# Performance work log

Measured on AMD Instinct MI355X. Metric: run time of the kernel, lower is better.

The kernel has to match this reference:

```python
import jax, jax.numpy as jnp
import numpy as np

N_NODES = 50000
N_EDGES = 1_600_000
D_IN, D_HID, D_OUT, K = 128, 50, 10, 5


def setup_inputs() -> dict:
    key = jax.random.key(0)
    ks = jax.random.split(key, 6)
    x = jax.random.normal(ks[0], (N_NODES, D_IN), dtype=jnp.float32)
    edge_index = jax.random.randint(ks[1], (2, N_EDGES), 0, N_NODES, dtype=jnp.int64)
    cheb_w = jax.random.normal(ks[2], (K, D_IN, D_HID), dtype=jnp.float32) * 0.05
    cheb_b = jax.random.normal(ks[3], (D_HID,), dtype=jnp.float32) * 0.05
    fc_w = jax.random.normal(ks[4], (D_HID, D_OUT), dtype=jnp.float32) * 0.1
    fc_b = jax.random.normal(ks[5], (D_OUT,), dtype=jnp.float32) * 0.1
    return {"x": x, "edge_index": edge_index, "cheb_w": cheb_w,
            "cheb_b": cheb_b, "fc_w": fc_w, "fc_b": fc_b}


def reference(x, edge_index, cheb_w, cheb_b, fc_w, fc_b):
    # ChebConv (PyG, normalization='sym', lambda_max=2.0):
    # L_hat = 2L/lambda_max - I = -D^{-1/2} A D^{-1/2} (zero diagonal)
    row, col = edge_index[0], edge_index[1]
    n = x.shape[0]
    deg = jax.ops.segment_sum(jnp.ones_like(row, dtype=x.dtype), row, num_segments=n)
    dinv = jnp.where(deg > 0, jax.lax.rsqrt(jnp.maximum(deg, 1.0)), 0.0)
    w = -dinv[row] * dinv[col]  # [E] edge weights of L_hat

    def prop(h):  # L_hat @ h via gather-scale-scatter
        return jax.ops.segment_sum(w[:, None] * h[col], row, num_segments=n)

    tx0 = x
    tx1 = prop(x)
    out = jnp.einsum('ni,io->no', tx0, cheb_w[0]) + jnp.einsum('ni,io->no', tx1, cheb_w[1])
    for k in range(2, K):
        tx2 = 2.0 * prop(tx1) - tx0
        out = out + jnp.einsum('ni,io->no', tx2, cheb_w[k])
        tx0, tx1 = tx1, tx2
    out = out + cheb_b

    h = jax.nn.relu(out)
    logits = h @ fc_w + fc_b
    return jax.nn.log_softmax(logits, axis=1)
```

## Files before the change

### kernel.cpp

```cpp
#include <hip/hip_runtime.h>
#include <hip/hip_fp16.h>

#define N_NODES 50000
#define N_EDGES 1600000
#define D_IN    128
#define D_HID   50
#define D_OUT   10
#define K_CHEB  5

#define WH_ELEMS  (K_CHEB * 64 * D_IN)
#define WH_BLOCKS ((WH_ELEMS + 255) / 256)
#define XH_BLOCKS (N_NODES * D_IN / 8 / 256)

#define P1S_BLOCKS 512
#define EPB        (N_EDGES / P1S_BLOCKS)
#define NBUCK      256
#define NB_USED    196
#define BCAP       48

#define VROW      64
#define VSTRIDE   ((size_t)(N_NODES + 1) * VROW)

#define NGROUP    (N_NODES / 16)
#define VG_SPAN   512
#define VG_WAVES  (K_CHEB * VG_SPAN)
#define VGB_BLOCKS (VG_WAVES / 8)

typedef _Float16 half8_t __attribute__((ext_vector_type(8)));
typedef float    f32x4_t __attribute__((ext_vector_type(4)));


__global__ __launch_bounds__(256) void buildA_kernel(const int* __restrict__ row,
                                                     const int* __restrict__ col,
                                                     unsigned int* __restrict__ store,
                                                     int* __restrict__ bcnt,
                                                     const float* __restrict__ x,
                                                     const float* __restrict__ W,
                                                     __half* __restrict__ xh,
                                                     __half* __restrict__ Wh,
                                                     __half* __restrict__ u,
                                                     __half* __restrict__ b1,
                                                     __half* __restrict__ b3,
                                                     __half* __restrict__ b2,
                                                     float* __restrict__ dinv) {
    __shared__ int cnt[NBUCK];
    int tid = threadIdx.x;
    int blk = blockIdx.x;
    if (blk < P1S_BLOCKS) {
        cnt[tid] = 0;
        __syncthreads();
        int base = blk * EPB;
        size_t sb = (size_t)blk * (NBUCK * BCAP);
        for (int i = tid; i < EPB; i += 256) {
            int r = row[base + i];
            int c = col[base + i];
            int b = r >> 8;
            int pos = atomicAdd(&cnt[b], 1);
            if (pos >= BCAP) pos = BCAP - 1;
            store[sb + b * BCAP + pos] = ((unsigned int)(r & 255) << 16) | (unsigned int)c;
        }
        __syncthreads();
        bcnt[blk * NBUCK + tid] = cnt[tid];
        return;
    }
    int pb = blk - P1S_BLOCKS;
    if (pb < XH_BLOCKS) {
        size_t base = ((size_t)pb * 256 + tid) * 8;
        float4 a = *(const float4*)(x + base);
        float4 b = *(const float4*)(x + base + 4);
        half8_t h;
        h[0] = (_Float16)a.x; h[1] = (_Float16)a.y;
        h[2] = (_Float16)a.z; h[3] = (_Float16)a.w;
        h[4] = (_Float16)b.x; h[5] = (_Float16)b.y;
        h[6] = (_Float16)b.z; h[7] = (_Float16)b.w;
        *(half8_t*)(xh + base) = h;
    } else if (pb < XH_BLOCKS + WH_BLOCKS) {
        int idx = (pb - XH_BLOCKS) * 256 + tid;
        if (idx < WH_ELEMS) {
            int i = idx & 127;
            int n = (idx >> 7) & 63;
            int t = idx >> 13;
            float vv = (n < D_HID) ? W[t * D_IN * D_HID + i * D_HID + n] : 0.f;
            Wh[idx] = __float2half(vv);
        }
    } else {
        if (tid < VROW) {
            __half z = __float2half(0.f);
            u[4 * VSTRIDE + (size_t)N_NODES * VROW + tid] = z;
            b1[(size_t)N_NODES * VROW + tid] = z;
            b3[(size_t)N_NODES * VROW + tid] = z;
            b2[(size_t)N_NODES * VROW + tid] = z;
        }
        if (tid == 64) dinv[N_NODES] = 0.f;
    }
}

__global__ __launch_bounds__(512) void buildB_kernel(const unsigned int* __restrict__ store,
                                                     const int* __restrict__ bcnt,
                                                     int* __restrict__ row_start,
                                                     float* __restrict__ dinv,
                                                     float* __restrict__ dinv2,
                                                     float* __restrict__ sdeg,
                                                     int* __restrict__ ewc,
                                                     const __half* __restrict__ xh,
                                                     const __half* __restrict__ Wh,
                                                     __half* __restrict__ u) {
    __shared__ int hist[256];
    __shared__ int off[256];
    __shared__ int fill[256];
    __shared__ int sb_part[512];
    __shared__ int pscan[256];
    __shared__ int s_bbase;
    int tid = threadIdx.x;
    int blk = blockIdx.x;
    if (blk >= NB_USED) {
        int lane = tid & 63;
        int wv = __builtin_amdgcn_readfirstlane(tid >> 6);
        int w = (blk - NB_USED) * 8 + wv;
        int t = w / VG_SPAN;
        int idx = w - t * VG_SPAN;
        int m = lane & 15;
        int quad = lane >> 4;

        const __half* Wt = Wh + t * (64 * D_IN);
        half8_t afr[4][4];
        #pragma unroll
        for (int ks = 0; ks < 4; ++ks) {
            int ko = ks * 32 + quad * 8;
            #pragma unroll
            for (int jt = 0; jt < 4; ++jt)
                afr[ks][jt] = *(const half8_t*)(Wt + (jt * 16 + m) * D_IN + ko);
        }

        __half* ut = u + t * VSTRIDE;

        half8_t pf[4];
        int g = idx;
        {
            const __half* xr = xh + (size_t)(g * 16 + m) * D_IN;
            #pragma unroll
            for (int ks = 0; ks < 4; ++ks)
                pf[ks] = *(const half8_t*)(xr + ks * 32 + quad * 8);
        }

        for (; g < NGROUP; g += VG_SPAN) {
            int node = g * 16 + m;
            half8_t bfr[4];
            #pragma unroll
            for (int ks = 0; ks < 4; ++ks) bfr[ks] = pf[ks];
            int gn = g + VG_SPAN;
            if (gn < NGROUP) {
                const __half* xr = xh + (size_t)(gn * 16 + m) * D_IN;
                #pragma unroll
                for (int ks = 0; ks < 4; ++ks)
                    pf[ks] = *(const half8_t*)(xr + ks * 32 + quad * 8);
            }
            f32x4_t acc[4];
            #pragma unroll
            for (int jt = 0; jt < 4; ++jt) acc[jt] = (f32x4_t)0.f;
            #pragma unroll
            for (int ks = 0; ks < 4; ++ks)
                #pragma unroll
                for (int jt = 0; jt < 4; ++jt)
                    acc[jt] = __builtin_amdgcn_mfma_f32_16x16x32_f16(afr[ks][jt], bfr[ks], acc[jt], 0, 0, 0);
            __half* dst = ut + (size_t)node * VROW + quad * 4;
            #pragma unroll
            for (int jt = 0; jt < 4; ++jt) {
                __half2 h0 = __float22half2_rn(make_float2(acc[jt][0], acc[jt][1]));
                __half2 h1 = __float22half2_rn(make_float2(acc[jt][2], acc[jt][3]));
                uint2 uu;
                uu.x = *(unsigned int*)&h0;
                uu.y = *(unsigned int*)&h1;
                *(uint2*)(dst + jt * 16) = uu;
            }
        }
        return;
    }
    int b = blk;
    {
        int bt = tid & 255, seg = tid >> 8;
        int sum = 0;
        for (int s = seg * 256; s < seg * 256 + 256; ++s) sum += bcnt[s * NBUCK + bt];
        sb_part[tid] = sum;
    }
    __syncthreads();
    if (tid < 256) pscan[tid] = sb_part[tid] + sb_part[256 + tid];
    __syncthreads();
    for (int o = 1; o < 256; o <<= 1) {
        int vv = (tid < 256 && tid >= o) ? pscan[tid - o] : 0;
        __syncthreads();
        if (tid < 256) pscan[tid] += vv;
        __syncthreads();
    }
    if (tid == 0) {
        s_bbase = (b == 0) ? 0 : pscan[b - 1];
        if (b == 0) row_start[N_NODES] = pscan[255];
    }
    if (tid < 256) hist[tid] = 0;
    __syncthreads();
    int bbase_b = s_bbase;

    int strip = tid;
    int sn = bcnt[strip * NBUCK + b];
    size_t sb = (size_t)strip * (NBUCK * BCAP) + b * BCAP;
    for (int i = 0; i < sn; ++i)
        atomicAdd(&hist[store[sb + i] >> 16], 1);
    __syncthreads();
    int d = (tid < 256) ? hist[tid] : 0;
    if (tid < 256) off[tid] = d;
    __syncthreads();
    for (int o = 1; o < 256; o <<= 1) {
        int vv = (tid < 256 && tid >= o) ? off[tid - o] : 0;
        __syncthreads();
        if (tid < 256) off[tid] += vv;
        __syncthreads();
    }
    if (tid < 256) {
        int excl = off[tid] - d + bbase_b;
        hist[tid] = excl;
        fill[tid] = 0;
        int r = (b << 8) + tid;
        if (r < N_NODES) {
            row_start[r] = excl;
            float fd = (float)d;
            dinv[r]  = d ? rsqrtf(fd)  : 0.f;
            dinv2[r] = d ? (1.f / fd)  : 0.f;
            sdeg[r]  = d ? sqrtf(fd)   : 0.f;
        }
    }
    __syncthreads();
    for (int i = 0; i < sn; ++i) {
        unsigned int vv = store[sb + i];
        int rl = vv >> 16;
        int c = vv & 0xffff;
        int p = atomicAdd(&fill[rl], 1);
        ewc[hist[rl] + p] = c;
    }
}

template<int SCALE_SRC, int DO_SUB, int SCALE_SUB>
__global__ __launch_bounds__(512) void prop_kernel(const int* __restrict__ row_start,
                                                   const int* __restrict__ ewc,
                                                   const float* __restrict__ dinv2,
                                                   const float* __restrict__ dinv,
                                                   const __half* __restrict__ src,
                                                   const __half* __restrict__ addv,
                                                   const __half* __restrict__ subv,
                                                   float alphaM,
                                                   __half* __restrict__ dst) {
    int tid = threadIdx.x;
    int lane = tid & 63;
    int wv = __builtin_amdgcn_readfirstlane(tid >> 6);
    int r = blockIdx.x * 8 + wv;
    int e0 = row_start[r], e1 = row_start[r + 1];
    float fac = -alphaM * dinv2[r];
    int l = lane & 7;
    int g = lane >> 3;
    const uint4* src16 = (const uint4*)src;
    float ac[8];
    #pragma unroll
    for (int j = 0; j < 8; ++j) ac[j] = 0.f;
    for (int e = e0; e < e1; e += 16) {
        #pragma unroll
        for (int i = 0; i < 2; ++i) {
            int base = e + 8 * i;
            int cl = ewc[base + g];
            if (base + g >= e1) cl = N_NODES;
            uint4 uu = src16[(size_t)cl * 8 + l];
            float2 f0 = __half22float2(*(__half2*)&uu.x);
            float2 f1 = __half22float2(*(__half2*)&uu.y);
            float2 f2 = __half22float2(*(__half2*)&uu.z);
            float2 f3 = __half22float2(*(__half2*)&uu.w);
            if (SCALE_SRC) {
                float dc = dinv[cl];
                ac[0] = fmaf(dc, f0.x, ac[0]); ac[1] = fmaf(dc, f0.y, ac[1]);
                ac[2] = fmaf(dc, f1.x, ac[2]); ac[3] = fmaf(dc, f1.y, ac[3]);
                ac[4] = fmaf(dc, f2.x, ac[4]); ac[5] = fmaf(dc, f2.y, ac[5]);
                ac[6] = fmaf(dc, f3.x, ac[6]); ac[7] = fmaf(dc, f3.y, ac[7]);
            } else {
                ac[0] += f0.x; ac[1] += f0.y; ac[2] += f1.x; ac[3] += f1.y;
                ac[4] += f2.x; ac[5] += f2.y; ac[6] += f3.x; ac[7] += f3.y;
            }
        }
    }
    #pragma unroll
    for (int k = 8; k <= 32; k <<= 1) {
        #pragma unroll
        for (int j = 0; j < 8; ++j) ac[j] += __shfl_xor(ac[j], k);
    }
    if (g == 0) {
        float sa = dinv[r];
        size_t o = (size_t)r * 8 + l;
        uint4 av = ((const uint4*)addv)[o];
        float2 av0 = __half22float2(*(__half2*)&av.x);
        float2 av1 = __half22float2(*(__half2*)&av.y);
        float2 av2 = __half22float2(*(__half2*)&av.z);
        float2 av3 = __half22float2(*(__half2*)&av.w);
        float r0 = fmaf(sa, av0.x, fac * ac[0]);
        float r1 = fmaf(sa, av0.y, fac * ac[1]);
        float r2 = fmaf(sa, av1.x, fac * ac[2]);
        float r3 = fmaf(sa, av1.y, fac * ac[3]);
        float r4 = fmaf(sa, av2.x, fac * ac[4]);
        float r5 = fmaf(sa, av2.y, fac * ac[5]);
        float r6 = fmaf(sa, av3.x, fac * ac[6]);
        float r7 = fmaf(sa, av3.y, fac * ac[7]);
        if (DO_SUB) {
            float ss = SCALE_SUB ? dinv[r] : 1.f;
            uint4 sv = ((const uint4*)subv)[o];
            float2 sv0 = __half22float2(*(__half2*)&sv.x);
            float2 sv1 = __half22float2(*(__half2*)&sv.y);
            float2 sv2 = __half22float2(*(__half2*)&sv.z);
            float2 sv3 = __half22float2(*(__half2*)&sv.w);
            r0 = fmaf(-ss, sv0.x, r0); r1 = fmaf(-ss, sv0.y, r1);
            r2 = fmaf(-ss, sv1.x, r2); r3 = fmaf(-ss, sv1.y, r3);
            r4 = fmaf(-ss, sv2.x, r4); r5 = fmaf(-ss, sv2.y, r5);
            r6 = fmaf(-ss, sv3.x, r6); r7 = fmaf(-ss, sv3.y, r7);
        }
        __half2 h0 = __float22half2_rn(make_float2(r0, r1));
        __half2 h1 = __float22half2_rn(make_float2(r2, r3));
        __half2 h2 = __float22half2_rn(make_float2(r4, r5));
        __half2 h3 = __float22half2_rn(make_float2(r6, r7));
        uint4 uu;
        uu.x = *(unsigned int*)&h0;
        uu.y = *(unsigned int*)&h1;
        uu.z = *(unsigned int*)&h2;
        uu.w = *(unsigned int*)&h3;
        ((uint4*)dst)[o] = uu;
    }
}

__global__ __launch_bounds__(256) void final_kernel(const __half* __restrict__ S,
                                                    const float* __restrict__ sdeg,
                                                    const float* __restrict__ cheb_b,
                                                    const float* __restrict__ fc_w,
                                                    const float* __restrict__ fc_b,
                                                    float* __restrict__ out) {
    int r = blockIdx.x * blockDim.x + threadIdx.x;
    if (r >= N_NODES) return;
    float sc = sdeg[r];
    const __half2* s2 = (const __half2*)(S + (size_t)r * VROW);
    float h[D_HID];
    #pragma unroll
    for (int i = 0; i < D_HID / 2; ++i) {
        float2 f = __half22float2(s2[i]);
        float v0 = sc * f.x + cheb_b[2 * i];
        float v1 = sc * f.y + cheb_b[2 * i + 1];
        h[2 * i]     = v0 > 0.f ? v0 : 0.f;
        h[2 * i + 1] = v1 > 0.f ? v1 : 0.f;
    }
    float lg[D_OUT];
    #pragma unroll
    for (int o = 0; o < D_OUT; ++o) lg[o] = fc_b[o];
    #pragma unroll 2
    for (int i = 0; i < D_HID; ++i) {
        float hv = h[i];
        #pragma unroll
        for (int o = 0; o < D_OUT; ++o) lg[o] += hv * fc_w[i * D_OUT + o];
    }
    float mx = lg[0];
    #pragma unroll
    for (int o = 1; o < D_OUT; ++o) mx = fmaxf(mx, lg[o]);
    float s = 0.f;
    #pragma unroll
    for (int o = 0; o < D_OUT; ++o) s += __expf(lg[o] - mx);
    float ls = __logf(s);
    size_t oo = (size_t)r * D_OUT;
    #pragma unroll
    for (int o = 0; o < D_OUT; ++o) out[oo + o] = lg[o] - mx - ls;
}

extern "C" void kernel_launch(void* const* d_in, const int* in_sizes, int n_in,
                              void* d_out, int out_size, void* d_ws, size_t ws_size,
                              hipStream_t stream) {
    const float* x      = (const float*)d_in[0];
    const int*   edge   = (const int*)d_in[1];
    const float* cheb_w = (const float*)d_in[2];
    const float* cheb_b = (const float*)d_in[3];
    const float* fc_w   = (const float*)d_in[4];
    const float* fc_b   = (const float*)d_in[5];
    float* out = (float*)d_out;

    const int* erow = edge;
    const int* ecol = edge + N_EDGES;

    uintptr_t p = ((uintptr_t)d_ws + 255) & ~(uintptr_t)255;
    auto alloc = [&](size_t bytes) {
        uintptr_t q = p;
        p = (p + bytes + 255) & ~(uintptr_t)255;
        return (void*)q;
    };
    int*    row_start = (int*)alloc((size_t)(N_NODES + 1) * 4);
    float*  dinv      = (float*)alloc((size_t)(N_NODES + 1) * 4);
    float*  dinv2     = (float*)alloc((size_t)N_NODES * 4);
    float*  sdeg      = (float*)alloc((size_t)N_NODES * 4);
    int*    ewc       = (int*)alloc((size_t)(N_EDGES + 32) * 4);
    unsigned int* store = (unsigned int*)alloc((size_t)P1S_BLOCKS * NBUCK * BCAP * 4);
    int*    bcnt      = (int*)alloc((size_t)P1S_BLOCKS * NBUCK * 4);
    __half* Wh        = (__half*)alloc((size_t)WH_ELEMS * 2);
    __half* xh        = (__half*)alloc((size_t)N_NODES * D_IN * 2);
    __half* Sbuf      = (__half*)alloc(VSTRIDE * 2);
    __half* u         = (__half*)alloc(5 * VSTRIDE * 2);
    __half* b1        = (__half*)alloc(VSTRIDE * 2);
    __half* b3        = (__half*)alloc(VSTRIDE * 2);
    __half* b2        = (__half*)alloc(VSTRIDE * 2);
    __half* S  = Sbuf;

    buildA_kernel<<<P1S_BLOCKS + XH_BLOCKS + WH_BLOCKS + 1, 256, 0, stream>>>(
        erow, ecol, store, bcnt, x, cheb_w, xh, Wh, u, b1, b3, b2, dinv);

    buildB_kernel<<<NB_USED + VGB_BLOCKS, 512, 0, stream>>>(
        store, bcnt, row_start, dinv, dinv2, sdeg, ewc, xh, Wh, u);

    __half* u0 = u;
    __half* u1 = u + 1 * VSTRIDE;
    __half* u2 = u + 2 * VSTRIDE;
    __half* u3 = u + 3 * VSTRIDE;
    __half* u4 = u + 4 * VSTRIDE;
    const int PB = N_NODES / 8;
    prop_kernel<1, 0, 0><<<PB, 512, 0, stream>>>(row_start, ewc, dinv2, dinv,
                                                 u4, u3, u3, 2.f, b3);
    prop_kernel<0, 1, 1><<<PB, 512, 0, stream>>>(row_start, ewc, dinv2, dinv,
                                                 b3, u2, u4, 2.f, b2);
    prop_kernel<0, 1, 0><<<PB, 512, 0, stream>>>(row_start, ewc, dinv2, dinv,
                                                 b2, u1, b3, 2.f, b1);
    prop_kernel<0, 1, 0><<<PB, 512, 0, stream>>>(row_start, ewc, dinv2, dinv,
                                                 b1, u0, b2, 1.f, S);

    final_kernel<<<(N_NODES + 255) / 256, 256, 0, stream>>>(S, sdeg, cheb_b,
                                                            fc_w, fc_b, out);
}
```

Before: 295.0 us.

## Fuse final MLP/log-softmax into last propagation and widen bucket-sort blocks

```diff
diff --git a/kernel.cpp b/kernel.cpp
--- a/kernel.cpp
+++ b/kernel.cpp
@@ -24,7 +24,7 @@
 #define NGROUP    (N_NODES / 16)
 #define VG_SPAN   512
 #define VG_WAVES  (K_CHEB * VG_SPAN)
-#define VGB_BLOCKS (VG_WAVES / 8)
+#define VGB_BLOCKS (VG_WAVES / 16)
 
 typedef _Float16 half8_t __attribute__((ext_vector_type(8)));
 typedef float    f32x4_t __attribute__((ext_vector_type(4)));
@@ -51,6 +51,7 @@
         __syncthreads();
         int base = blk * EPB;
         size_t sb = (size_t)blk * (NBUCK * BCAP);
+        #pragma unroll 2
         for (int i = tid; i < EPB; i += 256) {
             int r = row[base + i];
             int c = col[base + i];
@@ -95,20 +96,20 @@
     }
 }
 
-__global__ __launch_bounds__(512) void buildB_kernel(const unsigned int* __restrict__ store,
-                                                     const int* __restrict__ bcnt,
-                                                     int* __restrict__ row_start,
-                                                     float* __restrict__ dinv,
-                                                     float* __restrict__ dinv2,
-                                                     float* __restrict__ sdeg,
-                                                     int* __restrict__ ewc,
-                                                     const __half* __restrict__ xh,
-                                                     const __half* __restrict__ Wh,
-                                                     __half* __restrict__ u) {
+__global__ __launch_bounds__(1024) void buildB_kernel(const unsigned int* __restrict__ store,
+                                                      const int* __restrict__ bcnt,
+                                                      int* __restrict__ row_start,
+                                                      float* __restrict__ dinv,
+                                                      float* __restrict__ dinv2,
+                                                      float* __restrict__ sdeg,
+                                                      int* __restrict__ ewc,
+                                                      const __half* __restrict__ xh,
+                                                      const __half* __restrict__ Wh,
+                                                      __half* __restrict__ u) {
     __shared__ int hist[256];
     __shared__ int off[256];
     __shared__ int fill[256];
-    __shared__ int sb_part[512];
+    __shared__ int sb_part[1024];
     __shared__ int pscan[256];
     __shared__ int s_bbase;
     int tid = threadIdx.x;
@@ -116,7 +117,7 @@
     if (blk >= NB_USED) {
         int lane = tid & 63;
         int wv = __builtin_amdgcn_readfirstlane(tid >> 6);
-        int w = (blk - NB_USED) * 8 + wv;
+        int w = (blk - NB_USED) * 16 + wv;
         int t = w / VG_SPAN;
         int idx = w - t * VG_SPAN;
         int m = lane & 15;
@@ -180,11 +181,12 @@
     {
         int bt = tid & 255, seg = tid >> 8;
         int sum = 0;
-        for (int s = seg * 256; s < seg * 256 + 256; ++s) sum += bcnt[s * NBUCK + bt];
+        for (int s = seg * 128; s < seg * 128 + 128; ++s) sum += bcnt[s * NBUCK + bt];
         sb_part[tid] = sum;
     }
     __syncthreads();
-    if (tid < 256) pscan[tid] = sb_part[tid] + sb_part[256 + tid];
+    if (tid < 256) pscan[tid] = sb_part[tid] + sb_part[256 + tid]
+                              + sb_part[512 + tid] + sb_part[768 + tid];
     __syncthreads();
     for (int o = 1; o < 256; o <<= 1) {
         int vv = (tid < 256 && tid >= o) ? pscan[tid - o] : 0;
@@ -200,10 +202,11 @@
     __syncthreads();
     int bbase_b = s_bbase;
 
-    int strip = tid;
+    int strip = tid >> 1;
+    int sub   = tid & 1;
     int sn = bcnt[strip * NBUCK + b];
     size_t sb = (size_t)strip * (NBUCK * BCAP) + b * BCAP;
-    for (int i = 0; i < sn; ++i)
+    for (int i = sub; i < sn; i += 2)
         atomicAdd(&hist[store[sb + i] >> 16], 1);
     __syncthreads();
     int d = (tid < 256) ? hist[tid] : 0;
@@ -229,7 +232,7 @@
         }
     }
     __syncthreads();
-    for (int i = 0; i < sn; ++i) {
+    for (int i = sub; i < sn; i += 2) {
         unsigned int vv = store[sb + i];
         int rl = vv >> 16;
         int c = vv & 0xffff;
@@ -238,7 +241,7 @@
     }
 }
 
-template<int SCALE_SRC, int DO_SUB, int SCALE_SUB>
+template<int SCALE_SRC, int DO_SUB, int SCALE_SUB, int FINAL>
 __global__ __launch_bounds__(512) void prop_kernel(const int* __restrict__ row_start,
                                                    const int* __restrict__ ewc,
                                                    const float* __restrict__ dinv2,
@@ -247,7 +250,12 @@
                                                    const __half* __restrict__ addv,
                                                    const __half* __restrict__ subv,
                                                    float alphaM,
-                                                   __half* __restrict__ dst) {
+                                                   __half* __restrict__ dst,
+                                                   const float* __restrict__ sdeg,
+                                                   const float* __restrict__ cheb_b,
+                                                   const float* __restrict__ fc_w,
+                                                   const float* __restrict__ fc_b,
+                                                   float* __restrict__ out) {
     int tid = threadIdx.x;
     int lane = tid & 63;
     int wv = __builtin_amdgcn_readfirstlane(tid >> 6);
@@ -288,6 +296,69 @@
         #pragma unroll
         for (int j = 0; j < 8; ++j) ac[j] += __shfl_xor(ac[j], k);
     }
+
+    if (FINAL) {
+        float sa = dinv[r];
+        size_t o = (size_t)r * 8 + l;
+        uint4 av = ((const uint4*)addv)[o];
+        float2 av0 = __half22float2(*(__half2*)&av.x);
+        float2 av1 = __half22float2(*(__half2*)&av.y);
+        float2 av2 = __half22float2(*(__half2*)&av.z);
+        float2 av3 = __half22float2(*(__half2*)&av.w);
+        uint4 sv = ((const uint4*)subv)[o];
+        float2 sv0 = __half22float2(*(__half2*)&sv.x);
+        float2 sv1 = __half22float2(*(__half2*)&sv.y);
+        float2 sv2 = __half22float2(*(__half2*)&sv.z);
+        float2 sv3 = __half22float2(*(__half2*)&sv.w);
+        float rr[8];
+        rr[0] = fmaf(sa, av0.x, fac * ac[0]) - sv0.x;
+        rr[1] = fmaf(sa, av0.y, fac * ac[1]) - sv0.y;
+        rr[2] = fmaf(sa, av1.x, fac * ac[2]) - sv1.x;
+        rr[3] = fmaf(sa, av1.y, fac * ac[3]) - sv1.y;
+        rr[4] = fmaf(sa, av2.x, fac * ac[4]) - sv2.x;
+        rr[5] = fmaf(sa, av2.y, fac * ac[5]) - sv2.y;
+        rr[6] = fmaf(sa, av3.x, fac * ac[6]) - sv3.x;
+        rr[7] = fmaf(sa, av3.y, fac * ac[7]) - sv3.y;
+        float sc = sdeg[r];
+        int i0 = l * 8;
+        float lg[D_OUT];
+        #pragma unroll
+        for (int o2 = 0; o2 < D_OUT; ++o2) lg[o2] = 0.f;
+        #pragma unroll
+        for (int j = 0; j < 8; ++j) {
+            int i = i0 + j;
+            if (i < D_HID) {
+                float hv = fmaxf(fmaf(sc, rr[j], cheb_b[i]), 0.f);
+                #pragma unroll
+                for (int o2 = 0; o2 < D_OUT; ++o2)
+                    lg[o2] = fmaf(hv, fc_w[i * D_OUT + o2], lg[o2]);
+            }
+        }
+        #pragma unroll
+        for (int k = 1; k <= 4; k <<= 1) {
+            #pragma unroll
+            for (int o2 = 0; o2 < D_OUT; ++o2) lg[o2] += __shfl_xor(lg[o2], k);
+        }
+        #pragma unroll
+        for (int o2 = 0; o2 < D_OUT; ++o2) lg[o2] += fc_b[o2];
+        float mx = lg[0];
+        #pragma unroll
+        for (int o2 = 1; o2 < D_OUT; ++o2) mx = fmaxf(mx, lg[o2]);
+        float s = 0.f;
+        #pragma unroll
+        for (int o2 = 0; o2 < D_OUT; ++o2) s += __expf(lg[o2] - mx);
+        float sh = mx + __logf(s);
+        if (lane == 0) {
+            float* op = out + (size_t)r * D_OUT;
+            ((float2*)op)[0] = make_float2(lg[0] - sh, lg[1] - sh);
+            ((float2*)op)[1] = make_float2(lg[2] - sh, lg[3] - sh);
+            ((float2*)op)[2] = make_float2(lg[4] - sh, lg[5] - sh);
+            ((float2*)op)[3] = make_float2(lg[6] - sh, lg[7] - sh);
+            ((float2*)op)[4] = make_float2(lg[8] - sh, lg[9] - sh);
+        }
+        return;
+    }
+
     if (g == 0) {
         float sa = dinv[r];
         size_t o = (size_t)r * 8 + l;
@@ -329,46 +400,6 @@
     }
 }
 
-__global__ __launch_bounds__(256) void final_kernel(const __half* __restrict__ S,
-                                                    const float* __restrict__ sdeg,
-                                                    const float* __restrict__ cheb_b,
-                                                    const float* __restrict__ fc_w,
-                                                    const float* __restrict__ fc_b,
-                                                    float* __restrict__ out) {
-    int r = blockIdx.x * blockDim.x + threadIdx.x;
-    if (r >= N_NODES) return;
-    float sc = sdeg[r];
-    const __half2* s2 = (const __half2*)(S + (size_t)r * VROW);
-    float h[D_HID];
-    #pragma unroll
-    for (int i = 0; i < D_HID / 2; ++i) {
-        float2 f = __half22float2(s2[i]);
-        float v0 = sc * f.x + cheb_b[2 * i];
-        float v1 = sc * f.y + cheb_b[2 * i + 1];
-        h[2 * i]     = v0 > 0.f ? v0 : 0.f;
-        h[2 * i + 1] = v1 > 0.f ? v1 : 0.f;
-    }
-    float lg[D_OUT];
-    #pragma unroll
-    for (int o = 0; o < D_OUT; ++o) lg[o] = fc_b[o];
-    #pragma unroll 2
-    for (int i = 0; i < D_HID; ++i) {
-        float hv = h[i];
-        #pragma unroll
-        for (int o = 0; o < D_OUT; ++o) lg[o] += hv * fc_w[i * D_OUT + o];
-    }
-    float mx = lg[0];
-    #pragma unroll
-    for (int o = 1; o < D_OUT; ++o) mx = fmaxf(mx, lg[o]);
-    float s = 0.f;
-    #pragma unroll
-    for (int o = 0; o < D_OUT; ++o) s += __expf(lg[o] - mx);
-    float ls = __logf(s);
-    size_t oo = (size_t)r * D_OUT;
-    #pragma unroll
-    for (int o = 0; o < D_OUT; ++o) out[oo + o] = lg[o] - mx - ls;
-}
-
 extern "C" void kernel_launch(void* const* d_in, const int* in_sizes, int n_in,
                               void* d_out, int out_size, void* d_ws, size_t ws_size,
                               hipStream_t stream) {
@@ -398,17 +429,15 @@
     int*    bcnt      = (int*)alloc((size_t)P1S_BLOCKS * NBUCK * 4);
     __half* Wh        = (__half*)alloc((size_t)WH_ELEMS * 2);
     __half* xh        = (__half*)alloc((size_t)N_NODES * D_IN * 2);
-    __half* Sbuf      = (__half*)alloc(VSTRIDE * 2);
     __half* u         = (__half*)alloc(5 * VSTRIDE * 2);
     __half* b1        = (__half*)alloc(VSTRIDE * 2);
     __half* b3        = (__half*)alloc(VSTRIDE * 2);
     __half* b2        = (__half*)alloc(VSTRIDE * 2);
-    __half* S  = Sbuf;
 
     buildA_kernel<<<P1S_BLOCKS + XH_BLOCKS + WH_BLOCKS + 1, 256, 0, stream>>>(
         erow, ecol, store, bcnt, x, cheb_w, xh, Wh, u, b1, b3, b2, dinv);
 
-    buildB_kernel<<<NB_USED + VGB_BLOCKS, 512, 0, stream>>>(
+    buildB_kernel<<<NB_USED + VGB_BLOCKS, 1024, 0, stream>>>(
         store, bcnt, row_start, dinv, dinv2, sdeg, ewc, xh, Wh, u);
 
     __half* u0 = u;
@@ -417,15 +446,12 @@
     __half* u3 = u + 3 * VSTRIDE;
     __half* u4 = u + 4 * VSTRIDE;
     const int PB = N_NODES / 8;
-    prop_kernel<1, 0, 0><<<PB, 512, 0, stream>>>(row_start, ewc, dinv2, dinv,
-                                                 u4, u3, u3, 2.f, b3);
-    prop_kernel<0, 1, 1><<<PB, 512, 0, stream>>>(row_start, ewc, dinv2, dinv,
-                                                 b3, u2, u4, 2.f, b2);
-    prop_kernel<0, 1, 0><<<PB, 512, 0, stream>>>(row_start, ewc, dinv2, dinv,
-                                                 b2, u1, b3, 2.f, b1);
-    prop_kernel<0, 1, 0><<<PB, 512, 0, stream>>>(row_start, ewc, dinv2, dinv,
-                                                 b1, u0, b2, 1.f, S);
-
-    final_kernel<<<(N_NODES + 255) / 256, 256, 0, stream>>>(S, sdeg, cheb_b,
-                                                            fc_w, fc_b, out);
+    prop_kernel<1, 0, 0, 0><<<PB, 512, 0, stream>>>(row_start, ewc, dinv2, dinv,
+        u4, u3, u3, 2.f, b3, nullptr, nullptr, nullptr, nullptr, nullptr);
+    prop_kernel<0, 1, 1, 0><<<PB, 512, 0, stream>>>(row_start, ewc, dinv2, dinv,
+        b3, u2, u4, 2.f, b2, nullptr, nullptr, nullptr, nullptr, nullptr);
+    prop_kernel<0, 1, 0, 0><<<PB, 512, 0, stream>>>(row_start, ewc, dinv2, dinv,
+        b2, u1, b3, 2.f, b1, nullptr, nullptr, nullptr, nullptr, nullptr);
+    prop_kernel<0, 1, 0, 1><<<PB, 512, 0, stream>>>(row_start, ewc, dinv2, dinv,
+        b1, u0, b2, 1.f, nullptr, sdeg, cheb_b, fc_w, fc_b, out);
 }
```

Measured after the change: 340.8 us. 15.5% more time.
